# Optimization experiments

Hardware: AMD Instinct MI355X
Metric: run time of the kernel (lower is better)

## Reference

```python
import jax, jax.numpy as jnp
import numpy as np

BLK = 128          # block size for fp8 block-wise scales
FP8_MAX = 448.0    # max representable magnitude of float8_e4m3fn


def _dequant_act(a, s):
    # a: (E, M, K) fp8 values stored in fp32; s: (E, M, K//BLK) per-token 1x128 scales
    E, M, K = a.shape
    nb = K // BLK
    return (a.reshape(E, M, nb, BLK) * s[..., None]).reshape(E, M, K)


def _dequant_w(w, s):
    # w: (E, N, K) fp8 values stored in fp32; s: (E, N//BLK, K//BLK) 128x128 block scales
    E, N, K = w.shape
    return (w.reshape(E, N // BLK, BLK, K // BLK, BLK) * s[:, :, None, :, None]).reshape(E, N, K)


def _fp8_round(x):
    # round-to-fp8(e4m3fn) with straight-through value semantics
    q = x.astype(jnp.float8_e4m3fn).astype(jnp.float32)
    return x + jax.lax.stop_gradient(q - x)


def setup_inputs() -> dict:
    key = jax.random.key(0)
    ks = jax.random.split(key, 8)
    E, N, K, M = 8, 2048, 4096, 1024
    f8 = lambda x: x.astype(jnp.float8_e4m3fn).astype(jnp.float32)
    hidden_states_fp8 = f8(jax.random.normal(ks[0], (E, M, K), dtype=jnp.float32))
    hidden_states_scale = jax.random.uniform(ks[1], (E, M, K // BLK), dtype=jnp.float32, minval=0.01, maxval=1.0)
    masked_m = jax.random.randint(ks[2], (E,), 1, M + 1, dtype=jnp.int32)
    w13_weight_fp8 = f8(jax.random.normal(ks[3], (E, N, K), dtype=jnp.float32))
    w13_weight_scale = jax.random.uniform(ks[4], (E, N // BLK, K // BLK), dtype=jnp.float32, minval=0.01, maxval=1.0)
    w2_weight_fp8 = f8(jax.random.normal(ks[5], (E, K, N // 2), dtype=jnp.float32))
    w2_weight_scale = jax.random.uniform(ks[6], (E, K // BLK, N // 2 // BLK), dtype=jnp.float32, minval=0.01, maxval=1.0)
    return {
        "hidden_states_fp8": hidden_states_fp8,
        "hidden_states_scale": hidden_states_scale,
        "masked_m": masked_m,
        "expected_m": 512,
        "w13_weight_fp8": w13_weight_fp8,
        "w13_weight_scale": w13_weight_scale,
        "w2_weight_fp8": w2_weight_fp8,
        "w2_weight_scale": w2_weight_scale,
    }


def reference(hidden_states_fp8, hidden_states_scale, masked_m, expected_m,
              w13_weight_fp8, w13_weight_scale, w2_weight_fp8, w2_weight_scale):
    E, M, K = hidden_states_fp8.shape
    # per-expert row validity mask (rows >= masked_m[e] are padding)
    mask = jnp.arange(M)[None, :] < masked_m[:, None]            # (E, M)

    # --- grouped GEMM 1: (x @ w13^T) -> bf16, masked by valid rows ---
    a = _dequant_act(hidden_states_fp8, hidden_states_scale)     # (E, M, K)
    w13 = _dequant_w(w13_weight_fp8, w13_weight_scale)           # (E, N, K)
    gateup = jnp.einsum('emk,enk->emn', a, w13)
    gateup = gateup.astype(jnp.bfloat16).astype(jnp.float32)     # gemm emits bf16

    # --- fused SiLU * mul + per-128-block fp8 quantization ---
    gate, up = jnp.split(gateup, 2, axis=-1)                     # (E, M, N/2) each
    x = jax.nn.silu(gate) * up
    x = jnp.where(mask[..., None], x, 0.0)
    N2 = x.shape[-1]
    nb = N2 // BLK
    xb = x.reshape(E, M, nb, BLK)
    amax = jnp.max(jnp.abs(xb), axis=-1)                         # (E, M, nb)
    scale = jnp.maximum(amax, 1e-10) / FP8_MAX
    q = _fp8_round(xb / scale[..., None])                        # fp8-rounded values
    a2 = (q * scale[..., None]).reshape(E, M, N2)                # dequantized for gemm 2

    # --- grouped GEMM 2: (down_input @ w2^T) -> bf16 ---
    w2 = _dequant_w(w2_weight_fp8, w2_weight_scale)              # (E, K, N/2)
    out = jnp.einsum('emn,ekn->emk', a2, w2).astype(jnp.bfloat16)
    out = jnp.where(mask[..., None], out, jnp.bfloat16(0))
    return out
```

## Files before the change

### kernel.cpp

```cpp
#include <hip/hip_runtime.h>
#include <hip/hip_bf16.h>

#define E_  8
#define M_  1024
#define K_  4096
#define N_  2048
#define N2_ 1024

typedef unsigned short u16;
typedef unsigned char  u8;
typedef unsigned int   u32;
typedef long           i64;

typedef __bf16 bf16x8 __attribute__((ext_vector_type(8)));
typedef float  f32x4  __attribute__((ext_vector_type(4)));

union FragU { uint4 u; bf16x8 v; };

__device__ __forceinline__ u16 f2bfu(float f){
  union { __hip_bfloat16 h; u16 u; } c;
  c.h = __float2bfloat16(f);
  return c.u;
}
__device__ __forceinline__ u32 pack2(float a, float b){
  return (u32)f2bfu(a) | ((u32)f2bfu(b) << 16);
}
__device__ __forceinline__ float bf2f(u16 u){
  u32 x = ((u32)u) << 16;
  return __uint_as_float(x);
}
__device__ __forceinline__ float bf16val(float f){
  return bf2f(f2bfu(f));
}
__device__ __forceinline__ float fp8_round(float x){
  float ax = fabsf(x);
  if (ax < 0.015625f){
    return rintf(x * 512.0f) * (1.0f/512.0f);
  }
  u32 u = __float_as_uint(x);
  u32 lsb = (u >> 20) & 1u;
  u += 0x7FFFFu + lsb;
  u &= 0xFFF00000u;
  return __uint_as_float(u);
}
__device__ __forceinline__ u32 f2fp8(float v){
  u32 b = __float_as_uint(v);
  u32 s = (b >> 24) & 0x80u;
  int e = (int)((b >> 23) & 0xffu);
  u32 m = (b >> 20) & 7u;
  if (e >= 121) return s | ((u32)(e - 120) << 3) | m;
  return s | (u32)(fabsf(v) * 512.0f + 0.25f);
}

#define GLD16(g, l) __builtin_amdgcn_global_load_lds( \
    (const __attribute__((address_space(1))) void*)(g), \
    (__attribute__((address_space(3))) void*)(l), 16, 0, 0)

template<bool MASKED>
__global__ __launch_bounds__(256) void conv8_kernel(
    const float* __restrict__ src_, const int* __restrict__ masked_m,
    u8* __restrict__ dst)
{
  const int row = blockIdx.x, e = blockIdx.y;
  if (MASKED && row >= masked_m[e]) return;
  const int t = threadIdx.x;
  const size_t R = (size_t)e*gridDim.x + row;
  const float* s = src_ + R*K_ + t*16;
  const float4 f0 = *reinterpret_cast<const float4*>(s);
  const float4 f1 = *reinterpret_cast<const float4*>(s + 4);
  const float4 f2 = *reinterpret_cast<const float4*>(s + 8);
  const float4 f3 = *reinterpret_cast<const float4*>(s + 12);
  uint4 w;
  w.x = f2fp8(f0.x) | (f2fp8(f0.y)<<8) | (f2fp8(f0.z)<<16) | (f2fp8(f0.w)<<24);
  w.y = f2fp8(f1.x) | (f2fp8(f1.y)<<8) | (f2fp8(f1.z)<<16) | (f2fp8(f1.w)<<24);
  w.z = f2fp8(f2.x) | (f2fp8(f2.y)<<8) | (f2fp8(f2.z)<<16) | (f2fp8(f2.w)<<24);
  w.w = f2fp8(f3.x) | (f2fp8(f3.y)<<8) | (f2fp8(f3.z)<<16) | (f2fp8(f3.w)<<24);
  const int td = (t & ~7) | ((t & 7) ^ (row & 7));
  *reinterpret_cast<uint4*>(dst + R*K_ + td*16) = w;
}

__global__ __launch_bounds__(256, 2) void gemm1_fp8(
    const u8* __restrict__ A8, const float* __restrict__ Ascale,
    const u8* __restrict__ B8, const float* __restrict__ Wscale,
    const int* __restrict__ masked_m, u16* __restrict__ Cu)
{
  const int tn = blockIdx.x, tm = blockIdx.y, e = blockIdx.z;
  const int m0 = tm*128, n0 = tn*128;
  const int me = masked_m[e];
  if (m0 >= me) return;
  const int tid = threadIdx.x;
  const int lane = tid & 63, wid = tid >> 6;

  __shared__ u8 sA[2][128*128];
  __shared__ u8 sB[2][128*128];
  __shared__ float sSa[2][128];

  const size_t rbA = (size_t)e*M_ + m0;
  const size_t rbB = (size_t)e*N_ + n0;

  auto ISSUE = [&](const u8* G, size_t rowbase, int kt, u8* Sbuf){
    #pragma unroll
    for (int q = 0; q < 4; ++q){
      const int ins = wid*4 + q;
      const int r   = ins*8 + (lane >> 3);
      const u8* src = G + (rowbase + r)*K_ + kt*128 + (lane & 7)*16;
      GLD16(src, Sbuf + ins*1024);
    }
  };

  const int wm = wid >> 1, wn = wid & 1;
  const int fr = lane & 15, kg = lane >> 4;

  f32x4 acc[4][4];
  #pragma unroll
  for (int i = 0; i < 4; ++i)
    #pragma unroll
    for (int j = 0; j < 4; ++j)
      acc[i][j] = (f32x4){0.f, 0.f, 0.f, 0.f};

  auto COMPUTE = [&](int buf, float sw){
    f32x4 blk[4][4];
    #pragma unroll
    for (int ks = 0; ks < 4; ++ks){
      i64 av[4], bv[4];
      #pragma unroll
      for (int i = 0; i < 4; ++i){
        const int r   = wm*64 + i*16 + fr;
        const int c16 = ks*2 + (kg >> 1);
        const int ad  = r*128 + ((c16 ^ (r & 7)) << 4) + ((kg & 1) << 3);
        av[i] = *reinterpret_cast<const i64*>(&sA[buf][ad]);
      }
      #pragma unroll
      for (int j = 0; j < 4; ++j){
        const int r   = wn*64 + j*16 + fr;
        const int c16 = ks*2 + (kg >> 1);
        const int ad  = r*128 + ((c16 ^ (r & 7)) << 4) + ((kg & 1) << 3);
        bv[j] = *reinterpret_cast<const i64*>(&sB[buf][ad]);
      }
      #pragma unroll
      for (int i = 0; i < 4; ++i)
        #pragma unroll
        for (int j = 0; j < 4; ++j){
          f32x4 cin = (ks == 0) ? (f32x4){0.f,0.f,0.f,0.f} : blk[i][j];
          blk[i][j] = __builtin_amdgcn_mfma_f32_16x16x32_fp8_fp8(av[i], bv[j], cin, 0, 0, 0);
        }
    }
    #pragma unroll
    for (int i = 0; i < 4; ++i){
      f32x4 sa = *reinterpret_cast<const f32x4*>(&sSa[buf][wm*64 + i*16 + kg*4]);
      sa *= sw;
      #pragma unroll
      for (int j = 0; j < 4; ++j)
        acc[i][j] += sa * blk[i][j];
    }
  };

  float rSa = 0.f;
  if (tid < 128) rSa = Ascale[(rbA + tid)*32 + 0];
  ISSUE(A8, rbA, 0, sA[0]);
  ISSUE(B8, rbB, 0, sB[0]);
  if (tid < 128) sSa[0][tid] = rSa;
  asm volatile("s_waitcnt vmcnt(0) lgkmcnt(0)" ::: "memory");
  __builtin_amdgcn_s_barrier();
  __builtin_amdgcn_sched_barrier(0);

  int cur = 0;
  for (int kt = 0; kt < 32; ++kt){
    if (kt + 1 < 32){
      if (tid < 128) rSa = Ascale[(rbA + tid)*32 + kt + 1];
      ISSUE(A8, rbA, kt + 1, sA[cur ^ 1]);
      ISSUE(B8, rbB, kt + 1, sB[cur ^ 1]);
      if (tid < 128) sSa[cur ^ 1][tid] = rSa;
      asm volatile("s_waitcnt vmcnt(8)" ::: "memory");
    } else {
      asm volatile("s_waitcnt vmcnt(0)" ::: "memory");
    }
    __builtin_amdgcn_s_barrier();
    __builtin_amdgcn_sched_barrier(0);
    const float sw = Wscale[((size_t)e*16 + tn)*32 + kt];
    COMPUTE(cur, sw);
    asm volatile("s_waitcnt lgkmcnt(0)" ::: "memory");
    __builtin_amdgcn_s_barrier();
    __builtin_amdgcn_sched_barrier(0);
    cur ^= 1;
  }

  #pragma unroll
  for (int i = 0; i < 4; ++i){
    #pragma unroll
    for (int j = 0; j < 4; ++j){
      #pragma unroll
      for (int r = 0; r < 4; ++r){
        const int gm = m0 + wm*64 + i*16 + kg*4 + r;
        const int gn = n0 + wn*64 + j*16 + fr;
        if (gm < me) Cu[((size_t)e*M_ + gm)*N_ + gn] = f2bfu(acc[i][j][r]);
      }
    }
  }
}

template<int KD, int ND>
__global__ __launch_bounds__(256, 2) void gemm2_bf16(
    const u16* __restrict__ Abf, const float* __restrict__ Bptr,
    const float* __restrict__ Wscale, const int* __restrict__ masked_m,
    float* __restrict__ Cf)
{
  constexpr int BK  = 64;
  constexpr int KT  = KD / BK;
  constexpr int NKB = KD / 128;
  const int tn = blockIdx.x, tm = blockIdx.y, e = blockIdx.z;
  const int m0 = tm * 128, n0 = tn * 128;
  const int me = masked_m[e];
  const int tid = threadIdx.x;

  if (m0 >= me){
    const uint4 z = make_uint4(0u,0u,0u,0u);
    #pragma unroll
    for (int q = 0; q < 16; ++q){
      int idx = tid + 256*q;
      int r = idx >> 5, c = idx & 31;
      *reinterpret_cast<uint4*>(Cf + ((size_t)e*M_ + m0 + r)*ND + n0 + c*4) = z;
    }
    return;
  }

  __shared__ u16 sA[2][128*64];
  __shared__ u16 sB[2][128*64];

  const int lane = tid & 63, wid = tid >> 6;
  const int rrow = tid >> 3;
  const int kq   = tid & 7;

  float4 rB[8];
  float  sWv = 0.f;

  auto ISSUE_A = [&](int kt, int buf){
    const int k0 = kt * BK;
    #pragma unroll
    for (int q = 0; q < 4; ++q){
      const int ins = wid*4 + q;
      const int r   = ins*8 + (lane >> 3);
      const u16* src = Abf + ((size_t)e*M_ + m0 + r)*KD + k0 + (lane & 7)*8;
      GLD16(src, &sA[buf][ins*512]);
    }
  };
  auto LOAD_B = [&](int kt){
    const int k0 = kt * BK;
    const int kb = k0 >> 7;
    sWv = Wscale[((size_t)e*(ND/128) + tn)*NKB + kb];
    #pragma unroll
    for (int p = 0; p < 4; ++p){
      const int r = p*32 + rrow;
      const float* bp = Bptr + ((size_t)e*ND + n0 + r)*KD + k0 + kq*8;
      rB[2*p]   = *reinterpret_cast<const float4*>(bp);
      rB[2*p+1] = *reinterpret_cast<const float4*>(bp + 4);
    }
  };
  auto WRITE_B = [&](int buf){
    #pragma unroll
    for (int p = 0; p < 4; ++p){
      const int r   = p*32 + rrow;
      const int dst = r*64 + ((kq ^ (r & 7)) * 8);
      uint4 wb;
      wb.x = pack2(rB[2*p].x * sWv,   rB[2*p].y * sWv);
      wb.y = pack2(rB[2*p].z * sWv,   rB[2*p].w * sWv);
      wb.z = pack2(rB[2*p+1].x * sWv, rB[2*p+1].y * sWv);
      wb.w = pack2(rB[2*p+1].z * sWv, rB[2*p+1].w * sWv);
      *reinterpret_cast<uint4*>(&sB[buf][dst]) = wb;
    }
  };

  const int wm = wid >> 1, wn = wid & 1;
  const int fr = lane & 15, kg = lane >> 4;

  f32x4 acc[4][4];
  #pragma unroll
  for (int i = 0; i < 4; ++i)
    #pragma unroll
    for (int j = 0; j < 4; ++j)
      acc[i][j] = (f32x4){0.f, 0.f, 0.f, 0.f};

  auto COMPUTE = [&](int buf){
    #pragma unroll
    for (int ks = 0; ks < 2; ++ks){
      FragU av[4], bv[4];
      #pragma unroll
      for (int i = 0; i < 4; ++i){
        const int r  = wm*64 + i*16 + fr;
        const int ch = (ks*4 + kg) ^ (r & 7);
        av[i].u = *reinterpret_cast<const uint4*>(&sA[buf][r*64 + ch*8]);
      }
      #pragma unroll
      for (int j = 0; j < 4; ++j){
        const int r  = wn*64 + j*16 + fr;
        const int ch = (ks*4 + kg) ^ (r & 7);
        bv[j].u = *reinterpret_cast<const uint4*>(&sB[buf][r*64 + ch*8]);
      }
      #pragma unroll
      for (int i = 0; i < 4; ++i)
        #pragma unroll
        for (int j = 0; j < 4; ++j)
          acc[i][j] = __builtin_amdgcn_mfma_f32_16x16x32_bf16(av[i].v, bv[j].v, acc[i][j], 0, 0, 0);
    }
  };

  ISSUE_A(0, 0);
  LOAD_B(0);
  WRITE_B(0);
  __syncthreads();
  int cur = 0;
  for (int kt = 0; kt < KT; ++kt){
    if (kt + 1 < KT){
      ISSUE_A(kt + 1, cur ^ 1);
      LOAD_B(kt + 1);
    }
    COMPUTE(cur);
    if (kt + 1 < KT) WRITE_B(cur ^ 1);
    __syncthreads();
    cur ^= 1;
  }

  #pragma unroll
  for (int i = 0; i < 4; ++i){
    #pragma unroll
    for (int j = 0; j < 4; ++j){
      #pragma unroll
      for (int r = 0; r < 4; ++r){
        const int gm = m0 + wm*64 + i*16 + kg*4 + r;
        const int gn = n0 + wn*64 + j*16 + fr;
        const float v = (gm < me) ? bf16val(acc[i][j][r]) : 0.0f;
        Cf[((size_t)e*M_ + gm)*ND + gn] = v;
      }
    }
  }
}

__global__ __launch_bounds__(128) void act_quant_kernel(
    const u16* __restrict__ gu, const int* __restrict__ masked_m,
    u16* __restrict__ a2)
{
  const int m = blockIdx.x, e = blockIdx.y;
  if (m >= masked_m[e]) return;
  const int t = threadIdx.x;
  const u16* row = gu + ((size_t)e*M_ + m)*N_;
  uint4 g4 = *reinterpret_cast<const uint4*>(row + t*8);
  uint4 u4 = *reinterpret_cast<const uint4*>(row + N2_ + t*8);
  u32 gp[4] = {g4.x, g4.y, g4.z, g4.w};
  u32 up[4] = {u4.x, u4.y, u4.z, u4.w};

  float x[8];
  #pragma unroll
  for (int w = 0; w < 4; ++w){
    float g0 = bf2f((u16)(gp[w] & 0xffffu));
    float g1 = bf2f((u16)(gp[w] >> 16));
    float u0 = bf2f((u16)(up[w] & 0xffffu));
    float u1 = bf2f((u16)(up[w] >> 16));
    x[2*w]   = g0 / (1.0f + expf(-g0)) * u0;
    x[2*w+1] = g1 / (1.0f + expf(-g1)) * u1;
  }

  float amax = 0.f;
  #pragma unroll
  for (int k = 0; k < 8; ++k) amax = fmaxf(amax, fabsf(x[k]));
  #pragma unroll
  for (int o = 8; o > 0; o >>= 1) amax = fmaxf(amax, __shfl_xor(amax, o, 16));
  const float scale = fmaxf(amax, 1e-10f) / 448.0f;

  u32 hh[4];
  #pragma unroll
  for (int w = 0; w < 4; ++w){
    float d0 = fp8_round(x[2*w]   / scale) * scale;
    float d1 = fp8_round(x[2*w+1] / scale) * scale;
    hh[w] = pack2(d0, d1);
  }
  uint4 o4 = make_uint4(hh[0], hh[1], hh[2], hh[3]);
  const int td = (t & ~7) | ((t & 7) ^ (m & 7));
  *reinterpret_cast<uint4*>(a2 + ((size_t)e*M_ + m)*N2_ + td*8) = o4;
}

extern "C" void kernel_launch(void* const* d_in, const int* in_sizes, int n_in,
                              void* d_out, int out_size, void* d_ws, size_t ws_size,
                              hipStream_t stream)
{
  const float* hs   = (const float*)d_in[0];
  const float* hss  = (const float*)d_in[1];
  const int*   mm   = (const int*)d_in[2];
  const float* w13  = (const float*)d_in[4];
  const float* w13s = (const float*)d_in[5];
  const float* w2   = (const float*)d_in[6];
  const float* w2s  = (const float*)d_in[7];

  u16* gu    = (u16*)d_out;
  u8*  hs8   = (u8*)d_out + (size_t)E_*M_*N_*2;
  u8*  w13_8 = (u8*)d_out + (size_t)E_*M_*N_*2 + (size_t)E_*M_*K_;
  u16* a2    = (u16*)d_ws;

  conv8_kernel<true> <<<dim3(M_, E_), dim3(256), 0, stream>>>(hs,  mm, hs8);
  conv8_kernel<false><<<dim3(N_, E_), dim3(256), 0, stream>>>(w13, mm, w13_8);
  gemm1_fp8<<<dim3(N_/128, M_/128, E_), dim3(256), 0, stream>>>(
      hs8, hss, w13_8, w13s, mm, gu);
  act_quant_kernel<<<dim3(M_, E_), dim3(128), 0, stream>>>(gu, mm, a2);
  gemm2_bf16<N2_, K_><<<dim3(K_/128, M_/128, E_), dim3(256), 0, stream>>>(
      a2, w2, w2s, mm, (float*)d_out);
}
```

Before: 297.3 us.

## Remap GEMM workgroups across XCDs, preload all scales, add per-step MFMA priority

Both GEMMs now launch on a 1D grid and remap the block index so consecutive workgroups dispatched to the same XCD cover tiles of the same expert. This is meant to improve L2 reuse of shared A/B tiles. In gemm1, all 32 activation scales and weight scales for the tile are preloaded into shared memory once, which removes the per-iteration global scale loads. Each k-substep now waits on LDS reads, raises wave priority around the MFMA burst, and adds an extra barrier. That extra synchronisation may cost some overlap, and the scale preload adds shared memory, which may affect occupancy.

```diff
diff --git a/kernel.cpp b/kernel.cpp
--- a/kernel.cpp
+++ b/kernel.cpp
@@ -84,7 +84,10 @@
     const u8* __restrict__ B8, const float* __restrict__ Wscale,
     const int* __restrict__ masked_m, u16* __restrict__ Cu)
 {
-  const int tn = blockIdx.x, tm = blockIdx.y, e = blockIdx.z;
+  const int wg = ((blockIdx.x & 7) << 7) | (blockIdx.x >> 3);
+  const int e  = wg >> 7;
+  const int tm = (wg >> 4) & 7;
+  const int tn = wg & 15;
   const int m0 = tm*128, n0 = tn*128;
   const int me = masked_m[e];
   if (m0 >= me) return;
@@ -93,7 +96,8 @@
 
   __shared__ u8 sA[2][128*128];
   __shared__ u8 sB[2][128*128];
-  __shared__ float sSa[2][128];
+  __shared__ float sSaAll[32][128];
+  __shared__ float sSw[32];
 
   const size_t rbA = (size_t)e*M_ + m0;
   const size_t rbB = (size_t)e*N_ + n0;
@@ -118,7 +122,30 @@
     for (int j = 0; j < 4; ++j)
       acc[i][j] = (f32x4){0.f, 0.f, 0.f, 0.f};
 
-  auto COMPUTE = [&](int buf, float sw){
+  if (tid < 128){
+    const float* base = Ascale + (rbA + tid)*32;
+    #pragma unroll
+    for (int k = 0; k < 32; ++k) sSaAll[k][tid] = base[k];
+  }
+  if (tid < 32) sSw[tid] = Wscale[((size_t)e*16 + tn)*32 + tid];
+  ISSUE(A8, rbA, 0, sA[0]);
+  ISSUE(B8, rbB, 0, sB[0]);
+  asm volatile("s_waitcnt vmcnt(0) lgkmcnt(0)" ::: "memory");
+  __builtin_amdgcn_s_barrier();
+  __builtin_amdgcn_sched_barrier(0);
+
+  int cur = 0;
+  for (int kt = 0; kt < 32; ++kt){
+    if (kt + 1 < 32){
+      ISSUE(A8, rbA, kt + 1, sA[cur ^ 1]);
+      ISSUE(B8, rbB, kt + 1, sB[cur ^ 1]);
+      asm volatile("s_waitcnt vmcnt(8)" ::: "memory");
+    } else {
+      asm volatile("s_waitcnt vmcnt(0)" ::: "memory");
+    }
+    __builtin_amdgcn_s_barrier();
+    __builtin_amdgcn_sched_barrier(0);
+
     f32x4 blk[4][4];
     #pragma unroll
     for (int ks = 0; ks < 4; ++ks){
@@ -128,15 +155,18 @@
         const int r   = wm*64 + i*16 + fr;
         const int c16 = ks*2 + (kg >> 1);
         const int ad  = r*128 + ((c16 ^ (r & 7)) << 4) + ((kg & 1) << 3);
-        av[i] = *reinterpret_cast<const i64*>(&sA[buf][ad]);
+        av[i] = *reinterpret_cast<const i64*>(&sA[cur][ad]);
       }
       #pragma unroll
       for (int j = 0; j < 4; ++j){
         const int r   = wn*64 + j*16 + fr;
         const int c16 = ks*2 + (kg >> 1);
         const int ad  = r*128 + ((c16 ^ (r & 7)) << 4) + ((kg & 1) << 3);
-        bv[j] = *reinterpret_cast<const i64*>(&sB[buf][ad]);
-      }
+        bv[j] = *reinterpret_cast<const i64*>(&sB[cur][ad]);
+      }
+      asm volatile("s_waitcnt lgkmcnt(0)" ::: "memory");
+      __builtin_amdgcn_sched_barrier(0);
+      __builtin_amdgcn_s_setprio(1);
       #pragma unroll
       for (int i = 0; i < 4; ++i)
         #pragma unroll
@@ -144,44 +174,19 @@
           f32x4 cin = (ks == 0) ? (f32x4){0.f,0.f,0.f,0.f} : blk[i][j];
           blk[i][j] = __builtin_amdgcn_mfma_f32_16x16x32_fp8_fp8(av[i], bv[j], cin, 0, 0, 0);
         }
-    }
+      __builtin_amdgcn_s_setprio(0);
+      __builtin_amdgcn_s_barrier();
+    }
+
+    const float sw = sSw[kt];
     #pragma unroll
     for (int i = 0; i < 4; ++i){
-      f32x4 sa = *reinterpret_cast<const f32x4*>(&sSa[buf][wm*64 + i*16 + kg*4]);
+      f32x4 sa = *reinterpret_cast<const f32x4*>(&sSaAll[kt][wm*64 + i*16 + kg*4]);
       sa *= sw;
       #pragma unroll
       for (int j = 0; j < 4; ++j)
         acc[i][j] += sa * blk[i][j];
     }
-  };
-
-  float rSa = 0.f;
-  if (tid < 128) rSa = Ascale[(rbA + tid)*32 + 0];
-  ISSUE(A8, rbA, 0, sA[0]);
-  ISSUE(B8, rbB, 0, sB[0]);
-  if (tid < 128) sSa[0][tid] = rSa;
-  asm volatile("s_waitcnt vmcnt(0) lgkmcnt(0)" ::: "memory");
-  __builtin_amdgcn_s_barrier();
-  __builtin_amdgcn_sched_barrier(0);
-
-  int cur = 0;
-  for (int kt = 0; kt < 32; ++kt){
-    if (kt + 1 < 32){
-      if (tid < 128) rSa = Ascale[(rbA + tid)*32 + kt + 1];
-      ISSUE(A8, rbA, kt + 1, sA[cur ^ 1]);
-      ISSUE(B8, rbB, kt + 1, sB[cur ^ 1]);
-      if (tid < 128) sSa[cur ^ 1][tid] = rSa;
-      asm volatile("s_waitcnt vmcnt(8)" ::: "memory");
-    } else {
-      asm volatile("s_waitcnt vmcnt(0)" ::: "memory");
-    }
-    __builtin_amdgcn_s_barrier();
-    __builtin_amdgcn_sched_barrier(0);
-    const float sw = Wscale[((size_t)e*16 + tn)*32 + kt];
-    COMPUTE(cur, sw);
-    asm volatile("s_waitcnt lgkmcnt(0)" ::: "memory");
-    __builtin_amdgcn_s_barrier();
-    __builtin_amdgcn_sched_barrier(0);
     cur ^= 1;
   }
 
@@ -208,7 +213,10 @@
   constexpr int BK  = 64;
   constexpr int KT  = KD / BK;
   constexpr int NKB = KD / 128;
-  const int tn = blockIdx.x, tm = blockIdx.y, e = blockIdx.z;
+  const int wg = ((blockIdx.x & 7) << 8) | (blockIdx.x >> 3);
+  const int e  = wg >> 8;
+  const int tm = (wg >> 5) & 7;
+  const int tn = wg & 31;
   const int m0 = tm * 128, n0 = tn * 128;
   const int me = masked_m[e];
   const int tid = threadIdx.x;
@@ -397,9 +405,9 @@
 
   conv8_kernel<true> <<<dim3(M_, E_), dim3(256), 0, stream>>>(hs,  mm, hs8);
   conv8_kernel<false><<<dim3(N_, E_), dim3(256), 0, stream>>>(w13, mm, w13_8);
-  gemm1_fp8<<<dim3(N_/128, M_/128, E_), dim3(256), 0, stream>>>(
+  gemm1_fp8<<<dim3(1024), dim3(256), 0, stream>>>(
       hs8, hss, w13_8, w13s, mm, gu);
   act_quant_kernel<<<dim3(M_, E_), dim3(128), 0, stream>>>(gu, mm, a2);
-  gemm2_bf16<N2_, K_><<<dim3(K_/128, M_/128, E_), dim3(256), 0, stream>>>(
+  gemm2_bf16<N2_, K_><<<dim3(2048), dim3(256), 0, stream>>>(
       a2, w2, w2s, mm, (float*)d_out);
 }
```

After: 499.2 us. 67.9% more time.
